# Kernel optimization log

Hardware: AMD Instinct MI355X
Metric: run time of the kernel (lower is better)

The kernel has to match this reference:

```python
import jax, jax.numpy as jnp
import numpy as np

S, B, E, H, DFF = 1024, 4, 1024, 16, 4096
D = E // H  # head_dim = 64
EPS = 1e-5


def setup_inputs() -> dict:
    key = jax.random.key(0)
    ks = jax.random.split(key, 16)
    rn = lambda k, shape, s: jax.random.normal(k, shape, jnp.float32) * s
    # RoPE tables (half-rotation), theta=10000
    inv_freq = 1.0 / (10000.0 ** (jnp.arange(0, D, 2, dtype=jnp.float32) / D))  # [D/2]
    ang = jnp.arange(S, dtype=jnp.float32)[:, None] * inv_freq[None, :]          # [S, D/2]
    return {
        "q": rn(ks[0], (S, B, E), 1.0),
        "in_proj_w": rn(ks[1], (3 * E, E), E ** -0.5),
        "in_proj_b": rn(ks[2], (3 * E,), 0.02),
        "out_w": rn(ks[3], (E, E), E ** -0.5),
        "out_b": rn(ks[4], (E,), 0.02),
        "ln1_g": jnp.ones((E,), jnp.float32) + rn(ks[5], (E,), 0.02),
        "ln1_b": rn(ks[6], (E,), 0.02),
        "ln2_g": jnp.ones((E,), jnp.float32) + rn(ks[7], (E,), 0.02),
        "ln2_b": rn(ks[8], (E,), 0.02),
        "ff1_w": rn(ks[9], (DFF, E), E ** -0.5),
        "ff1_b": rn(ks[10], (DFF,), 0.02),
        "ff2_w": rn(ks[11], (E, DFF), DFF ** -0.5),
        "ff2_b": rn(ks[12], (E,), 0.02),
        "rope_cos": jnp.cos(ang),
        "rope_sin": jnp.sin(ang),
    }


def _layernorm(x, g, b):
    mu = jnp.mean(x, -1, keepdims=True)
    var = jnp.mean((x - mu) ** 2, -1, keepdims=True)
    return (x - mu) * jax.lax.rsqrt(var + EPS) * g + b


def reference(q, in_proj_w, in_proj_b, out_w, out_b, ln1_g, ln1_b, ln2_g, ln2_b,
              ff1_w, ff1_b, ff2_w, ff2_b, rope_cos, rope_sin):
    s, b, e = q.shape
    d = 2 * rope_cos.shape[-1]
    h = e // d
    # pre-norm (self-attention: k = v = q, so norm computed once)
    xq = _layernorm(q, ln1_g, ln1_b)
    # fused QKV projection
    qkv = xq @ in_proj_w.T + in_proj_b            # [s, b, 3e]
    qh, kh, vh = jnp.split(qkv, 3, axis=-1)
    qh = qh.reshape(s, b, h, d)
    kh = kh.reshape(s, b, h, d)
    vh = vh.reshape(s, b, h, d)

    def rope(t):
        t1, t2 = jnp.split(t, 2, axis=-1)          # [s, b, h, d/2] each
        c = rope_cos[:, None, None, :]
        sn = rope_sin[:, None, None, :]
        return jnp.concatenate([t1 * c - t2 * sn, t1 * sn + t2 * c], axis=-1)

    qh = rope(qh)
    kh = rope(kh)
    # attention (ssmax='none' -> identity scaling, dropout=0, no masks)
    scores = jnp.einsum("sbhd,tbhd->bhst", qh, kh) / jnp.sqrt(jnp.float32(d))
    attn = jax.nn.softmax(scores, axis=-1)
    ao = jnp.einsum("bhst,tbhd->sbhd", attn, vh).reshape(s, b, e)
    ao = ao @ out_w.T + out_b
    # residual + pre-norm FFN
    x = q + ao
    y = _layernorm(x, ln2_g, ln2_b)
    ff = jax.nn.gelu(y @ ff1_w.T + ff1_b, approximate=False) @ ff2_w.T + ff2_b
    return x + ff
```

## Files before the change

### kernel.cpp

```cpp
#include <hip/hip_runtime.h>
#include <hip/hip_bf16.h>
#include <stdint.h>

typedef float f32x4 __attribute__((ext_vector_type(4)));
typedef __bf16 bf16x8 __attribute__((ext_vector_type(8)));

__device__ __forceinline__ unsigned short f2bf(float f) {
    union { float f; unsigned u; } v; v.f = f;
    unsigned r = v.u + 0x7fffu + ((v.u >> 16) & 1u);
    return (unsigned short)(r >> 16);
}
__device__ __forceinline__ float bf2f(unsigned short u) {
    union { unsigned u; float f; } v; v.u = ((unsigned)u) << 16;
    return v.f;
}
__device__ __forceinline__ unsigned cvt_pk_bf16(float lo, float hi) {
    unsigned r;
    asm("v_cvt_pk_bf16_f32 %0, %1, %2" : "=v"(r) : "v"(lo), "v"(hi));
    return r;
}

__device__ __forceinline__ void gl_lds16(const void* g, void* l) {
    __builtin_amdgcn_global_load_lds(
        (const __attribute__((address_space(1))) void*)(unsigned long long)(uintptr_t)g,
        (__attribute__((address_space(3))) void*)(unsigned)(uintptr_t)l,
        16, 0, 0);
}

__global__ __launch_bounds__(256) void cvt_kernel(const float* __restrict__ in,
                                                  unsigned short* __restrict__ outp) {
    int i = blockIdx.x * 256 + threadIdx.x;
    float4 v = ((const float4*)in)[i];
    ushort4 o;
    o.x = f2bf(v.x); o.y = f2bf(v.y); o.z = f2bf(v.z); o.w = f2bf(v.w);
    ((ushort4*)outp)[i] = o;
}

__global__ __launch_bounds__(256) void ln_kernel(const float* __restrict__ x,
                                                 const float* __restrict__ g,
                                                 const float* __restrict__ b,
                                                 unsigned short* __restrict__ outp) {
    const int row = blockIdx.x;
    const int t = threadIdx.x;
    const float4 v = ((const float4*)(x + (size_t)row * 1024))[t];
    float s = v.x + v.y + v.z + v.w;
    float s2 = v.x * v.x + v.y * v.y + v.z * v.z + v.w * v.w;
    #pragma unroll
    for (int off = 1; off < 64; off <<= 1) {
        s  += __shfl_xor(s, off);
        s2 += __shfl_xor(s2, off);
    }
    __shared__ float red[8];
    const int w = t >> 6;
    if ((t & 63) == 0) { red[w * 2] = s; red[w * 2 + 1] = s2; }
    __syncthreads();
    s  = red[0] + red[2] + red[4] + red[6];
    s2 = red[1] + red[3] + red[5] + red[7];
    const float mu = s * (1.0f / 1024.0f);
    const float var = s2 * (1.0f / 1024.0f) - mu * mu;
    const float rstd = rsqrtf(var + 1e-5f);
    const float4 gv = ((const float4*)g)[t];
    const float4 bv = ((const float4*)b)[t];
    ushort4 o;
    o.x = f2bf((v.x - mu) * rstd * gv.x + bv.x);
    o.y = f2bf((v.y - mu) * rstd * gv.y + bv.y);
    o.z = f2bf((v.z - mu) * rstd * gv.z + bv.z);
    o.w = f2bf((v.w - mu) * rstd * gv.w + bv.w);
    ((ushort4*)(outp + (size_t)row * 1024))[t] = o;
}

__global__ __launch_bounds__(512) void rope_kernel(const unsigned short* __restrict__ qkv,
                                                   const float* __restrict__ rc,
                                                   const float* __restrict__ rs,
                                                   unsigned short* __restrict__ Qr,
                                                   unsigned short* __restrict__ Kr) {
    const int sb = blockIdx.x;
    const int s = sb >> 2, b = sb & 3;
    const int t = threadIdx.x;
    const int h = t >> 5, d = t & 31;
    const size_t rowo = (size_t)sb * 3072;
    const float c = rc[s * 32 + d];
    const float sn = rs[s * 32 + d];
    const size_t ho = ((size_t)(b * 16 + h) * 1024 + s) * 64;

    const float q1 = bf2f(qkv[rowo + h * 64 + d]);
    const float q2 = bf2f(qkv[rowo + h * 64 + d + 32]);
    Qr[ho + d]      = f2bf((q1 * c - q2 * sn) * 0.125f);
    Qr[ho + d + 32] = f2bf((q1 * sn + q2 * c) * 0.125f);

    const float k1 = bf2f(qkv[rowo + 1024 + h * 64 + d]);
    const float k2 = bf2f(qkv[rowo + 1024 + h * 64 + d + 32]);
    Kr[ho + d]      = f2bf(k1 * c - k2 * sn);
    Kr[ho + d + 32] = f2bf(k1 * sn + k2 * c);
}

__global__ __launch_bounds__(256) void vt_kernel(const unsigned short* __restrict__ qkv,
                                                 unsigned short* __restrict__ Vt) {
    __shared__ unsigned short t[64][66];
    const int s0 = blockIdx.x * 64;
    const int bh = blockIdx.y;
    const int b = bh >> 4, h = bh & 15;
    const int tid = threadIdx.x;
    const int si = tid >> 3, c = (tid & 7) * 8;
    #pragma unroll
    for (int r = 0; r < 2; r++) {
        const int s = si + r * 32;
        union { uint4 u; unsigned short sh[8]; } v;
        v.u = *(const uint4*)&qkv[((size_t)(s0 + s) * 4 + b) * 3072 + 2048 + h * 64 + c];
        #pragma unroll
        for (int i = 0; i < 8; i++) t[c + i][s] = v.sh[i];
    }
    __syncthreads();
    #pragma unroll
    for (int r = 0; r < 2; r++) {
        const int d = si + r * 32;
        const unsigned* rp = (const unsigned*)((const char*)&t[0][0] + d * 132 + c * 2);
        uint4 ov;
        ov.x = rp[0]; ov.y = rp[1]; ov.z = rp[2]; ov.w = rp[3];
        *(uint4*)&Vt[((size_t)bh * 64 + d) * 1024 + s0 + c] = ov;
    }
}

template <int EPI, int BM, int BN, int WM, int WN, bool CM>
__global__ __launch_bounds__((BM / WM) * (BN / WN) * 64, 2)
void gemm2(const unsigned short* __restrict__ A, const unsigned short* __restrict__ Bw,
           const float* __restrict__ bias, const float* __restrict__ res,
           void* __restrict__ Cout, int N, int K, int nbx) {
    constexpr int WAVES_N = BN / WN;
    constexpr int THREADS = (BM / WM) * (BN / WN) * 64;
    constexpr int MR = WM / 16, NR = WN / 16;
    constexpr int ASZ = BM * 64, BSZ = BN * 64;
    constexpr int RPP = THREADS / 8;
    __shared__ __attribute__((aligned(16))) unsigned short As[2 * ASZ];
    __shared__ __attribute__((aligned(16))) unsigned short Bs[2 * BSZ];

    const int nwg = gridDim.x;
    const int swz = (blockIdx.x & 7) * (nwg >> 3) + (blockIdx.x >> 3);
    const int nby = nwg / nbx;
    const int bx = CM ? (swz / nby) : (swz % nbx);
    const int by = CM ? (swz % nby) : (swz / nbx);
    const int bm = by * BM, bn = bx * BN;

    const int tid = threadIdx.x;
    const int w = tid >> 6, l = tid & 63;
    const int wr = w / WAVES_N, wc = w % WAVES_N;
    const int lm = l & 15, lg = l >> 4, lx = lm & 7;

    const int srow = tid >> 3;
    const int sgx = ((tid & 7) ^ (srow & 7)) * 8;
    const unsigned short* Ag = A + (size_t)(bm + srow) * K + sgx;
    const unsigned short* Bg = Bw + (size_t)(bn + srow) * K + sgx;

    const int c0 = ((lg ^ lx) << 3);
    const int c1 = (((4 + lg) ^ lx) << 3);

    f32x4 acc[MR][NR];
    #pragma unroll
    for (int i = 0; i < MR; i++)
        #pragma unroll
        for (int j = 0; j < NR; j++) acc[i][j] = f32x4{0.f, 0.f, 0.f, 0.f};

    auto STAGE = [&](int buf, int k0) {
        #pragma unroll
        for (int i = 0; i < BM / RPP; i++)
            gl_lds16(Ag + (size_t)i * RPP * K + k0, &As[buf * ASZ + i * RPP * 64 + tid * 8]);
        #pragma unroll
        for (int i = 0; i < BN / RPP; i++)
            gl_lds16(Bg + (size_t)i * RPP * K + k0, &Bs[buf * BSZ + i * RPP * 64 + tid * 8]);
    };

    STAGE(0, 0);
    asm volatile("s_waitcnt vmcnt(0)" ::: "memory");
    __syncthreads();

    const int NT = K >> 6;
    int cur = 0;
    for (int t = 0; t < NT; ++t) {
        if (t + 1 < NT) STAGE(cur ^ 1, (t + 1) << 6);
        const int ab = cur * ASZ, bb = cur * BSZ;
        #pragma unroll
        for (int h = 0; h < 2; h++) {
            const int cc = h ? c1 : c0;
            bf16x8 af[MR], bfr[NR];
            #pragma unroll
            for (int mi = 0; mi < MR; mi++)
                af[mi] = *(const bf16x8*)&As[ab + (wr * WM + mi * 16 + lm) * 64 + cc];
            #pragma unroll
            for (int ni = 0; ni < NR; ni++)
                bfr[ni] = *(const bf16x8*)&Bs[bb + (wc * WN + ni * 16 + lm) * 64 + cc];
            __builtin_amdgcn_s_setprio(1);
            #pragma unroll
            for (int mi = 0; mi < MR; mi++)
                #pragma unroll
                for (int ni = 0; ni < NR; ni++)
                    acc[mi][ni] = __builtin_amdgcn_mfma_f32_16x16x32_bf16(
                        af[mi], bfr[ni], acc[mi][ni], 0, 0, 0);
            __builtin_amdgcn_s_setprio(0);
        }
        asm volatile("s_waitcnt vmcnt(0)" ::: "memory");
        __syncthreads();
        cur ^= 1;
    }

    const int r0 = bm + wr * WM + lg * 4;
    #pragma unroll
    for (int ni = 0; ni < NR; ni++) {
        const int col = bn + wc * WN + ni * 16 + lm;
        const float bc = bias[col];
        #pragma unroll
        for (int mi = 0; mi < MR; mi++) {
            #pragma unroll
            for (int j = 0; j < 4; j++) {
                const int row = r0 + mi * 16 + j;
                const size_t idx = (size_t)row * N + col;
                const float v = acc[mi][ni][j] + bc;
                if constexpr (EPI == 0) {
                    ((unsigned short*)Cout)[idx] = f2bf(v);
                } else if constexpr (EPI == 1) {
                    ((float*)Cout)[idx] = v + res[idx];
                } else if constexpr (EPI == 2) {
                    const float ge = 0.5f * v * (1.0f + erff(v * 0.70710678118654752f));
                    ((unsigned short*)Cout)[idx] = f2bf(ge);
                } else {
                    ((float*)Cout)[idx] = v + res[idx];
                }
            }
        }
    }
}

__global__ __launch_bounds__(256, 4)
void attn_kernel(const unsigned short* __restrict__ Qr, const unsigned short* __restrict__ Kr,
                 const unsigned short* __restrict__ Vt, unsigned short* __restrict__ AO) {
    __shared__ __attribute__((aligned(16))) unsigned short Ks[64][72];
    __shared__ __attribute__((aligned(16))) unsigned short Vs[64][72];
    const int tid = threadIdx.x;
    const int w = tid >> 6, l = tid & 63;
    const int lm = l & 15, lg = l >> 4;
    const int qt = blockIdx.x, bh = blockIdx.y;
    const size_t hoff = (size_t)bh * (1024 * 64);

    const size_t qrow = hoff + (size_t)(qt * 64 + w * 16 + lm) * 64;
    const bf16x8 qf0 = *(const bf16x8*)&Qr[qrow + lg * 8];
    const bf16x8 qf1 = *(const bf16x8*)&Qr[qrow + 32 + lg * 8];

    float m = -1e30f, lsum = 0.f;
    f32x4 acc[4];
    #pragma unroll
    for (int i = 0; i < 4; i++) acc[i] = f32x4{0.f, 0.f, 0.f, 0.f};

    const int sr = tid >> 3, scc = (tid & 7) * 8;
    const int srcA = lm + 16 * ((2 * lg) & 3);
    const int srcB = lm + 16 * ((2 * lg + 1) & 3);
    const bool hi2 = (lg & 2) != 0;

    uint4 kr0 = *(const uint4*)&Kr[hoff + (size_t)sr * 64 + scc];
    uint4 kr1 = *(const uint4*)&Kr[hoff + (size_t)(sr + 32) * 64 + scc];
    uint4 vr0 = *(const uint4*)&Vt[hoff + (size_t)sr * 1024 + scc];
    uint4 vr1 = *(const uint4*)&Vt[hoff + (size_t)(sr + 32) * 1024 + scc];

    for (int kt = 0; kt < 16; kt++) {
        __syncthreads();
        *(uint4*)&Ks[sr][scc]      = kr0;
        *(uint4*)&Ks[sr + 32][scc] = kr1;
        *(uint4*)&Vs[sr][scc]      = vr0;
        *(uint4*)&Vs[sr + 32][scc] = vr1;
        __syncthreads();
        if (kt < 15) {
            const size_t kb = hoff + (size_t)(kt + 1) * 64 * 64;
            kr0 = *(const uint4*)&Kr[kb + (size_t)sr * 64 + scc];
            kr1 = *(const uint4*)&Kr[kb + (size_t)(sr + 32) * 64 + scc];
            vr0 = *(const uint4*)&Vt[hoff + (size_t)sr * 1024 + (kt + 1) * 64 + scc];
            vr1 = *(const uint4*)&Vt[hoff + (size_t)(sr + 32) * 1024 + (kt + 1) * 64 + scc];
        }

        f32x4 st[4];
        #pragma unroll
        for (int nt = 0; nt < 4; nt++) {
            const bf16x8 kf0 = *(const bf16x8*)&Ks[nt * 16 + lm][lg * 8];
            const bf16x8 kf1 = *(const bf16x8*)&Ks[nt * 16 + lm][32 + lg * 8];
            f32x4 s = f32x4{0.f, 0.f, 0.f, 0.f};
            s = __builtin_amdgcn_mfma_f32_16x16x32_bf16(kf0, qf0, s, 0, 0, 0);
            s = __builtin_amdgcn_mfma_f32_16x16x32_bf16(kf1, qf1, s, 0, 0, 0);
            st[nt] = s;
        }

        float tmax = st[0][0];
        #pragma unroll
        for (int nt = 0; nt < 4; nt++)
            #pragma unroll
            for (int j = 0; j < 4; j++) tmax = fmaxf(tmax, st[nt][j]);
        tmax = fmaxf(tmax, __shfl_xor(tmax, 16));
        tmax = fmaxf(tmax, __shfl_xor(tmax, 32));

        const float mnew = fmaxf(m, tmax);
        const float fac = __builtin_amdgcn_exp2f((m - mnew) * 1.4426950408889634f);
        m = mnew;

        unsigned pd[4][2];
        float rsum = 0.f;
        #pragma unroll
        for (int nt = 0; nt < 4; nt++) {
            const float p0 = __builtin_amdgcn_exp2f((st[nt][0] - mnew) * 1.4426950408889634f);
            const float p1 = __builtin_amdgcn_exp2f((st[nt][1] - mnew) * 1.4426950408889634f);
            const float p2 = __builtin_amdgcn_exp2f((st[nt][2] - mnew) * 1.4426950408889634f);
            const float p3 = __builtin_amdgcn_exp2f((st[nt][3] - mnew) * 1.4426950408889634f);
            rsum += (p0 + p1) + (p2 + p3);
            pd[nt][0] = cvt_pk_bf16(p0, p1);
            pd[nt][1] = cvt_pk_bf16(p2, p3);
        }
        rsum += __shfl_xor(rsum, 16);
        rsum += __shfl_xor(rsum, 32);
        lsum = lsum * fac + rsum;
        #pragma unroll
        for (int nt2 = 0; nt2 < 4; nt2++)
            #pragma unroll
            for (int j = 0; j < 4; j++) acc[nt2][j] *= fac;

        #pragma unroll
        for (int kt2 = 0; kt2 < 2; kt2++) {
            const int a0 = __shfl((int)pd[kt2 * 2][0], srcA);
            const int a1 = __shfl((int)pd[kt2 * 2 + 1][0], srcA);
            const int a2 = __shfl((int)pd[kt2 * 2][1], srcA);
            const int a3 = __shfl((int)pd[kt2 * 2 + 1][1], srcA);
            const int b0 = __shfl((int)pd[kt2 * 2][0], srcB);
            const int b1 = __shfl((int)pd[kt2 * 2 + 1][0], srcB);
            const int b2 = __shfl((int)pd[kt2 * 2][1], srcB);
            const int b3 = __shfl((int)pd[kt2 * 2 + 1][1], srcB);
            union { int u[4]; bf16x8 v; } pf;
            pf.u[0] = hi2 ? a1 : a0;
            pf.u[1] = hi2 ? a3 : a2;
            pf.u[2] = hi2 ? b1 : b0;
            pf.u[3] = hi2 ? b3 : b2;
            #pragma unroll
            for (int nt2 = 0; nt2 < 4; nt2++) {
                const bf16x8 vf = *(const bf16x8*)&Vs[nt2 * 16 + lm][kt2 * 32 + lg * 8];
                acc[nt2] = __builtin_amdgcn_mfma_f32_16x16x32_bf16(vf, pf.v, acc[nt2], 0, 0, 0);
            }
        }
    }

    const int b = bh >> 4, h = bh & 15;
    const float inv = 1.0f / lsum;
    const int s = qt * 64 + w * 16 + lm;
    #pragma unroll
    for (int nt2 = 0; nt2 < 4; nt2++) {
        ushort4 o;
        o.x = f2bf(acc[nt2][0] * inv);
        o.y = f2bf(acc[nt2][1] * inv);
        o.z = f2bf(acc[nt2][2] * inv);
        o.w = f2bf(acc[nt2][3] * inv);
        *(ushort4*)&AO[(size_t)(s * 4 + b) * 1024 + h * 64 + nt2 * 16 + lg * 4] = o;
    }
}

extern "C" void kernel_launch(void* const* d_in, const int* in_sizes, int n_in,
                              void* d_out, int out_size, void* d_ws, size_t ws_size,
                              hipStream_t stream) {
    const float* q    = (const float*)d_in[0];
    const float* w_in = (const float*)d_in[1];
    const float* b_in = (const float*)d_in[2];
    const float* w_o  = (const float*)d_in[3];
    const float* b_o  = (const float*)d_in[4];
    const float* g1   = (const float*)d_in[5];
    const float* be1  = (const float*)d_in[6];
    const float* g2   = (const float*)d_in[7];
    const float* be2  = (const float*)d_in[8];
    const float* w1   = (const float*)d_in[9];
    const float* b1   = (const float*)d_in[10];
    const float* w2   = (const float*)d_in[11];
    const float* b2   = (const float*)d_in[12];
    const float* rc   = (const float*)d_in[13];
    const float* rsn  = (const float*)d_in[14];
    float* outp = (float*)d_out;

    char* base = (char*)d_ws;
    if (ws_size < 109051904ull) return;

    unsigned short* wb_in  = (unsigned short*)(base + 0);
    unsigned short* wb_out = wb_in + 3145728;
    unsigned short* wb_ff1 = wb_out + 1048576;
    unsigned short* wb_ff2 = wb_ff1 + 4194304;
    unsigned short* xq  = (unsigned short*)(base + 25165824);
    unsigned short* qkv = (unsigned short*)(base + 33554432);
    unsigned short* hh  = (unsigned short*)(base + 33554432);
    unsigned short* Qr  = (unsigned short*)(base + 58720256);
    unsigned short* Kr  = (unsigned short*)(base + 67108864);
    unsigned short* Vt  = (unsigned short*)(base + 75497472);
    unsigned short* ao  = (unsigned short*)(base + 83886080);
    float*          x   = (float*)(base + 92274688);
    unsigned short* y   = xq;

    cvt_kernel<<<3072, 256, 0, stream>>>(w_in, wb_in);
    cvt_kernel<<<1024, 256, 0, stream>>>(w_o, wb_out);
    cvt_kernel<<<4096, 256, 0, stream>>>(w1, wb_ff1);
    cvt_kernel<<<4096, 256, 0, stream>>>(w2, wb_ff2);

    ln_kernel<<<4096, 256, 0, stream>>>(q, g1, be1, xq);
    gemm2<0, 128, 128, 64, 64, false><<<768, 256, 0, stream>>>(xq, wb_in, b_in, nullptr, qkv, 3072, 1024, 24);
    rope_kernel<<<4096, 512, 0, stream>>>(qkv, rc, rsn, Qr, Kr);
    vt_kernel<<<dim3(16, 64), 256, 0, stream>>>(qkv, Vt);
    attn_kernel<<<dim3(16, 64), 256, 0, stream>>>(Qr, Kr, Vt, ao);
    gemm2<1, 128, 128, 64, 64, true><<<256, 256, 0, stream>>>(ao, wb_out, b_o, q, x, 1024, 1024, 8);
    ln_kernel<<<4096, 256, 0, stream>>>(x, g2, be2, y);
    gemm2<2, 256, 256, 128, 64, false><<<256, 512, 0, stream>>>(y, wb_ff1, b1, nullptr, hh, 4096, 1024, 16);
    gemm2<3, 128, 128, 64, 64, true><<<256, 256, 0, stream>>>(hh, wb_ff2, b2, x, outp, 1024, 4096, 8);
}
```

Before: 248.2 us.

## Replace double-buffered swizzled GEMM with single-buffer kernel and retune tile configs

Rewrites the GEMM kernel to use a single LDS buffer with plain row-major layout instead of a double-buffered, XOR-swizzled prefetch pipeline, and raises the occupancy hint to three blocks per CU. The out-projection and FF2 GEMMs switch to 64x128 tiles with more blocks, and FF1 drops from 256x256 to 128x128 tiles. The aim is higher occupancy and more parallelism, at the cost of losing load/compute overlap and risking LDS bank conflicts from the unswizzled layout.

```diff
diff --git a/kernel.cpp b/kernel.cpp
--- a/kernel.cpp
+++ b/kernel.cpp
@@ -122,17 +122,14 @@
 }
 
 template <int EPI, int BM, int BN, int WM, int WN, bool CM>
-__global__ __launch_bounds__((BM / WM) * (BN / WN) * 64, 2)
-void gemm2(const unsigned short* __restrict__ A, const unsigned short* __restrict__ Bw,
-           const float* __restrict__ bias, const float* __restrict__ res,
-           void* __restrict__ Cout, int N, int K, int nbx) {
+__global__ __launch_bounds__(256, 3)
+void gemm97(const unsigned short* __restrict__ A, const unsigned short* __restrict__ Bw,
+            const float* __restrict__ bias, const float* __restrict__ res,
+            void* __restrict__ Cout, int N, int K, int nbx) {
     constexpr int WAVES_N = BN / WN;
-    constexpr int THREADS = (BM / WM) * (BN / WN) * 64;
     constexpr int MR = WM / 16, NR = WN / 16;
-    constexpr int ASZ = BM * 64, BSZ = BN * 64;
-    constexpr int RPP = THREADS / 8;
-    __shared__ __attribute__((aligned(16))) unsigned short As[2 * ASZ];
-    __shared__ __attribute__((aligned(16))) unsigned short Bs[2 * BSZ];
+    __shared__ __attribute__((aligned(16))) unsigned short As[BM * 64];
+    __shared__ __attribute__((aligned(16))) unsigned short Bs[BN * 64];
 
     const int nwg = gridDim.x;
     const int swz = (blockIdx.x & 7) * (nwg >> 3) + (blockIdx.x >> 3);
@@ -144,15 +141,12 @@
     const int tid = threadIdx.x;
     const int w = tid >> 6, l = tid & 63;
     const int wr = w / WAVES_N, wc = w % WAVES_N;
-    const int lm = l & 15, lg = l >> 4, lx = lm & 7;
+    const int lm = l & 15, lk = (l >> 4) * 8;
 
     const int srow = tid >> 3;
-    const int sgx = ((tid & 7) ^ (srow & 7)) * 8;
-    const unsigned short* Ag = A + (size_t)(bm + srow) * K + sgx;
-    const unsigned short* Bg = Bw + (size_t)(bn + srow) * K + sgx;
-
-    const int c0 = ((lg ^ lx) << 3);
-    const int c1 = (((4 + lg) ^ lx) << 3);
+    const int scol = (tid & 7) * 8;
+    const unsigned short* Ag = A + (size_t)(bm + srow) * K + scol;
+    const unsigned short* Bg = Bw + (size_t)(bn + srow) * K + scol;
 
     f32x4 acc[MR][NR];
     #pragma unroll
@@ -160,49 +154,34 @@
         #pragma unroll
         for (int j = 0; j < NR; j++) acc[i][j] = f32x4{0.f, 0.f, 0.f, 0.f};
 
-    auto STAGE = [&](int buf, int k0) {
-        #pragma unroll
-        for (int i = 0; i < BM / RPP; i++)
-            gl_lds16(Ag + (size_t)i * RPP * K + k0, &As[buf * ASZ + i * RPP * 64 + tid * 8]);
-        #pragma unroll
-        for (int i = 0; i < BN / RPP; i++)
-            gl_lds16(Bg + (size_t)i * RPP * K + k0, &Bs[buf * BSZ + i * RPP * 64 + tid * 8]);
-    };
-
-    STAGE(0, 0);
-    asm volatile("s_waitcnt vmcnt(0)" ::: "memory");
-    __syncthreads();
-
-    const int NT = K >> 6;
-    int cur = 0;
-    for (int t = 0; t < NT; ++t) {
-        if (t + 1 < NT) STAGE(cur ^ 1, (t + 1) << 6);
-        const int ab = cur * ASZ, bb = cur * BSZ;
-        #pragma unroll
-        for (int h = 0; h < 2; h++) {
-            const int cc = h ? c1 : c0;
+    for (int k0 = 0; k0 < K; k0 += 64) {
+        __syncthreads();
+        #pragma unroll
+        for (int i = 0; i < BM / 32; i++)
+            gl_lds16(Ag + (size_t)i * 32 * K + k0, &As[(srow + i * 32) * 64 + scol]);
+        #pragma unroll
+        for (int i = 0; i < BN / 32; i++)
+            gl_lds16(Bg + (size_t)i * 32 * K + k0, &Bs[(srow + i * 32) * 64 + scol]);
+        __syncthreads();
+        #pragma unroll
+        for (int kk = 0; kk < 64; kk += 32) {
             bf16x8 af[MR], bfr[NR];
             #pragma unroll
             for (int mi = 0; mi < MR; mi++)
-                af[mi] = *(const bf16x8*)&As[ab + (wr * WM + mi * 16 + lm) * 64 + cc];
+                af[mi] = *(const bf16x8*)&As[(wr * WM + mi * 16 + lm) * 64 + kk + lk];
             #pragma unroll
             for (int ni = 0; ni < NR; ni++)
-                bfr[ni] = *(const bf16x8*)&Bs[bb + (wc * WN + ni * 16 + lm) * 64 + cc];
-            __builtin_amdgcn_s_setprio(1);
+                bfr[ni] = *(const bf16x8*)&Bs[(wc * WN + ni * 16 + lm) * 64 + kk + lk];
             #pragma unroll
             for (int mi = 0; mi < MR; mi++)
                 #pragma unroll
                 for (int ni = 0; ni < NR; ni++)
                     acc[mi][ni] = __builtin_amdgcn_mfma_f32_16x16x32_bf16(
                         af[mi], bfr[ni], acc[mi][ni], 0, 0, 0);
-            __builtin_amdgcn_s_setprio(0);
-        }
-        asm volatile("s_waitcnt vmcnt(0)" ::: "memory");
-        __syncthreads();
-        cur ^= 1;
-    }
-
-    const int r0 = bm + wr * WM + lg * 4;
+        }
+    }
+
+    const int r0 = bm + wr * WM + (l >> 4) * 4;
     #pragma unroll
     for (int ni = 0; ni < NR; ni++) {
         const int col = bn + wc * WN + ni * 16 + lm;
@@ -397,12 +376,12 @@
     cvt_kernel<<<4096, 256, 0, stream>>>(w2, wb_ff2);
 
     ln_kernel<<<4096, 256, 0, stream>>>(q, g1, be1, xq);
-    gemm2<0, 128, 128, 64, 64, false><<<768, 256, 0, stream>>>(xq, wb_in, b_in, nullptr, qkv, 3072, 1024, 24);
+    gemm97<0, 128, 128, 64, 64, false><<<768, 256, 0, stream>>>(xq, wb_in, b_in, nullptr, qkv, 3072, 1024, 24);
     rope_kernel<<<4096, 512, 0, stream>>>(qkv, rc, rsn, Qr, Kr);
     vt_kernel<<<dim3(16, 64), 256, 0, stream>>>(qkv, Vt);
     attn_kernel<<<dim3(16, 64), 256, 0, stream>>>(Qr, Kr, Vt, ao);
-    gemm2<1, 128, 128, 64, 64, true><<<256, 256, 0, stream>>>(ao, wb_out, b_o, q, x, 1024, 1024, 8);
+    gemm97<1, 64, 128, 32, 64, true><<<512, 256, 0, stream>>>(ao, wb_out, b_o, q, x, 1024, 1024, 8);
     ln_kernel<<<4096, 256, 0, stream>>>(x, g2, be2, y);
-    gemm2<2, 256, 256, 128, 64, false><<<256, 512, 0, stream>>>(y, wb_ff1, b1, nullptr, hh, 4096, 1024, 16);
-    gemm2<3, 128, 128, 64, 64, true><<<256, 256, 0, stream>>>(hh, wb_ff2, b2, x, outp, 1024, 4096, 8);
-}
+    gemm97<2, 128, 128, 64, 64, false><<<1024, 256, 0, stream>>>(y, wb_ff1, b1, nullptr, hh, 4096, 1024, 32);
+    gemm97<3, 64, 128, 32, 64, true><<<512, 256, 0, stream>>>(hh, wb_ff2, b2, x, outp, 1024, 4096, 8);
+}
```

After: 277.7 us. 11.9% more time.
